# Performance work log

Hardware: AMD Instinct MI355X
Metric: run time of the kernel (lower is better)

The kernel has to match this reference:

```python
import jax, jax.numpy as jnp
import numpy as np

N = 250000   # num nodes
E = 250000   # num edges (tree: ~one parent per node)
D = 128      # embed_size
H = 256      # MLP hidden
HOPS = 3


def _mlp(x, w1, b1, w2, b2):
    # Sequential(Linear, ReLU, Linear, ReLU, Dropout(eval=identity))
    return jax.nn.relu(jnp.dot(jax.nn.relu(jnp.dot(x, w1) + b1), w2) + b2)


def _scatter_mean(src, idx, n):
    s = jax.ops.segment_sum(src, idx, num_segments=n)
    c = jax.ops.segment_sum(jnp.ones((src.shape[0],), src.dtype), idx, num_segments=n)
    return s / jnp.maximum(c, 1.0)[:, None]


def setup_inputs() -> dict:
    key = jax.random.key(0)
    ks = jax.random.split(key, 32)
    u = lambda k, shp: jax.random.uniform(k, shp, jnp.float32, -0.1, 0.1)
    inp = {
        "batch_token": jax.random.normal(ks[0], (N, D), jnp.float32),
        "self_idx_batch": jax.random.randint(ks[1], (E,), 0, N),
        "parent_idx_batch": jax.random.randint(ks[2], (E,), 0, N),
        "root_mask": (jax.random.uniform(ks[3], (N,)) < 0.01).astype(jnp.float32),
        "leaf_mask": (jax.random.uniform(ks[4], (N,)) < 0.3).astype(jnp.float32),
        "start_token": jax.random.normal(ks[5], (D,), jnp.float32),
        "end_token": jax.random.normal(ks[6], (D,), jnp.float32),
        # MLP_V: D -> H -> D
        "Vw1": u(ks[7], (D, H)), "Vb1": u(ks[8], (H,)), "Vw2": u(ks[9], (H, D)), "Vb2": u(ks[10], (D,)),
        # MLP_E: 1 -> H -> D
        "Ew1": u(ks[11], (1, H)), "Eb1": u(ks[12], (H,)), "Ew2": u(ks[13], (H, D)), "Eb2": u(ks[14], (D,)),
        # MLP_p: 3D -> H -> D
        "Pw1": u(ks[15], (3 * D, H)), "Pb1": u(ks[16], (H,)), "Pw2": u(ks[17], (H, D)), "Pb2": u(ks[18], (D,)),
        # MLP_c: 3D -> H -> D
        "Cw1": u(ks[19], (3 * D, H)), "Cb1": u(ks[20], (H,)), "Cw2": u(ks[21], (H, D)), "Cb2": u(ks[22], (D,)),
        # MLP_aggr: 3D -> H -> D
        "Aw1": u(ks[23], (3 * D, H)), "Ab1": u(ks[24], (H,)), "Aw2": u(ks[25], (H, D)), "Ab2": u(ks[26], (D,)),
    }
    return inp


def reference(batch_token, self_idx_batch, parent_idx_batch, root_mask, leaf_mask,
              start_token, end_token,
              Vw1, Vb1, Vw2, Vb2,
              Ew1, Eb1, Ew2, Eb2,
              Pw1, Pb1, Pw2, Pb2,
              Cw1, Cb1, Cw2, Cb2,
              Aw1, Ab1, Aw2, Ab2):
    n = batch_token.shape[0]
    edge_in = _mlp(jnp.ones((1, 1), batch_token.dtype), Ew1, Eb1, Ew2, Eb2)   # [1,D]
    edge_out = _mlp(jnp.zeros((1, 1), batch_token.dtype), Ew1, Eb1, Ew2, Eb2)  # [1,D]
    e = self_idx_batch.shape[0]
    edge_in = jnp.broadcast_to(edge_in, (e, edge_in.shape[1]))
    edge_out = jnp.broadcast_to(edge_out, (e, edge_out.shape[1]))

    hidden = _mlp(batch_token, Vw1, Vb1, Vw2, Vb2)  # [N,D]
    for _ in range(HOPS):
        node_self = hidden[self_idx_batch]      # [E,D] gather
        node_parent = hidden[parent_idx_batch]  # [E,D] gather
        inp_parent = jnp.concatenate([node_parent, node_self, edge_out], axis=-1)  # [E,3D]
        inp_child = jnp.concatenate([node_self, node_parent, edge_in], axis=-1)    # [E,3D]
        S_p = _mlp(inp_parent, Pw1, Pb1, Pw2, Pb2)
        S_c = _mlp(inp_child, Cw1, Cb1, Cw2, Cb2)
        S_p = _scatter_mean(S_p, self_idx_batch, n)
        S_c = _scatter_mean(S_c, parent_idx_batch, n)
        S_p = S_p + root_mask[:, None] * start_token
        S_c = S_c + leaf_mask[:, None] * end_token
        x_aggr = jnp.concatenate([hidden, S_p, S_c], axis=-1)  # [N,3D]
        hidden = hidden + _mlp(x_aggr, Aw1, Ab1, Aw2, Ab2)
    return hidden
```

## Files before the change

### kernel.cpp

```cpp
#include <hip/hip_runtime.h>

typedef __attribute__((ext_vector_type(8))) short short8;
typedef __attribute__((ext_vector_type(4))) float f32x4;

#define DD 128
#define HH 256

__device__ __forceinline__ unsigned short f2bf(float f) {
  unsigned int u = __float_as_uint(f);
  u += 0x7fffu + ((u >> 16) & 1u);
  return (unsigned short)(u >> 16);
}
__device__ __forceinline__ float bf2f(unsigned short s) {
  return __uint_as_float(((unsigned int)s) << 16);
}
__device__ __forceinline__ f32x4 mfma16(short8 a, short8 b, f32x4 c) {
  return __builtin_amdgcn_mfma_f32_16x16x32_bf16(a, b, c, 0, 0, 0);
}

__global__ void wconv(const float* __restrict__ src, unsigned short* __restrict__ dst,
                      int K, int Nout, int kswap) {
  int id = blockIdx.x * 256 + threadIdx.x;
  if (id >= K * Nout) return;
  int n = id / K, k = id - n * K;
  int ks = k + kswap; if (ks >= K) ks -= K;
  dst[n * K + k] = f2bf(src[(size_t)ks * Nout + n]);
}

__global__ void prep_bias(const float* __restrict__ Ew1, const float* __restrict__ Eb1,
                          const float* __restrict__ Ew2, const float* __restrict__ Eb2,
                          const float* __restrict__ Pw1, const float* __restrict__ Pb1,
                          const float* __restrict__ Cw1, const float* __restrict__ Cb1,
                          float* __restrict__ b1P, float* __restrict__ b1C) {
  __shared__ float h1[HH], h0[HH], ein[DD], eout[DD];
  int t = threadIdx.x;
  h1[t] = fmaxf(Ew1[t] + Eb1[t], 0.f);
  h0[t] = fmaxf(Eb1[t], 0.f);
  __syncthreads();
  if (t < DD) {
    float s1 = Eb2[t], s0 = Eb2[t];
    for (int j = 0; j < HH; ++j) { s1 += h1[j] * Ew2[j * DD + t]; s0 += h0[j] * Ew2[j * DD + t]; }
    ein[t]  = fmaxf(s1, 0.f);
    eout[t] = fmaxf(s0, 0.f);
  }
  __syncthreads();
  float bp = Pb1[t], bc = Cb1[t];
  for (int d = 0; d < DD; ++d) {
    bp += eout[d] * Pw1[(size_t)(256 + d) * HH + t];
    bc += ein[d]  * Cw1[(size_t)(256 + d) * HH + t];
  }
  b1P[t] = bp; b1C[t] = bc;
}

__global__ void count_k(const int* __restrict__ selfI, const int* __restrict__ parI,
                        int* degP, int* degC, int E) {
  int id = blockIdx.x * 256 + threadIdx.x;
  if (id < E) { atomicAdd(&degP[selfI[id]], 1); atomicAdd(&degC[parI[id]], 1); }
}

__global__ void scan1(const int* __restrict__ src, int* __restrict__ dst,
                      int* __restrict__ part, int n) {
  __shared__ int sh[256];
  int t = threadIdx.x;
  int base = blockIdx.x * 1024 + t * 4;
  int v0 = base + 0 < n ? src[base + 0] : 0;
  int v1 = base + 1 < n ? src[base + 1] : 0;
  int v2 = base + 2 < n ? src[base + 2] : 0;
  int v3 = base + 3 < n ? src[base + 3] : 0;
  int tsum = v0 + v1 + v2 + v3;
  sh[t] = tsum;
  __syncthreads();
  for (int off = 1; off < 256; off <<= 1) {
    int y = (t >= off) ? sh[t - off] : 0;
    __syncthreads();
    if (t >= off) sh[t] += y;
    __syncthreads();
  }
  int ex = sh[t] - tsum;
  if (base + 0 < n) dst[base + 0] = ex;
  if (base + 1 < n) dst[base + 1] = ex + v0;
  if (base + 2 < n) dst[base + 2] = ex + v0 + v1;
  if (base + 3 < n) dst[base + 3] = ex + v0 + v1 + v2;
  if (t == 255) part[blockIdx.x] = sh[255];
}

__global__ void scan2(int* __restrict__ part, int m) {
  __shared__ int sh[256];
  int t = threadIdx.x;
  int carry = 0;
  for (int base = 0; base < m; base += 256) {
    int v = (base + t < m) ? part[base + t] : 0;
    sh[t] = v;
    __syncthreads();
    for (int off = 1; off < 256; off <<= 1) {
      int y = (t >= off) ? sh[t - off] : 0;
      __syncthreads();
      if (t >= off) sh[t] += y;
      __syncthreads();
    }
    if (base + t < m) part[base + t] = carry + sh[t] - v;
    int tot = sh[255];
    __syncthreads();
    carry += tot;
  }
}

__global__ void scan3(int* __restrict__ dst, const int* __restrict__ part, int n) {
  int i = blockIdx.x * 256 + threadIdx.x;
  if (i < n) dst[i] += part[i >> 10];
}

__global__ void copy2(const int* __restrict__ a, int* __restrict__ b,
                      const int* __restrict__ c, int* __restrict__ d, int n) {
  int i = blockIdx.x * 256 + threadIdx.x;
  if (i < n) { b[i] = a[i]; d[i] = c[i]; }
}

__global__ void pos_k(const int* __restrict__ selfI, const int* __restrict__ parI,
                      int* curP, int* curC, int* posP, int* posC, int E) {
  int e = blockIdx.x * 256 + threadIdx.x;
  if (e < E) {
    posP[e] = atomicAdd(&curP[selfI[e]], 1);
    posC[e] = atomicAdd(&curC[parI[e]], 1);
  }
}

__global__ __launch_bounds__(512, 4) void v_kernel(
    const float* __restrict__ x, const unsigned short* __restrict__ W1t,
    const unsigned short* __restrict__ W2t, const float* __restrict__ b1,
    const float* __restrict__ b2, float* __restrict__ hidden,
    unsigned short* __restrict__ hbf, int n) {
  __shared__ __align__(16) unsigned short A[64 * 136];
  __shared__ __align__(16) unsigned short O1[64 * 264];
  int t = threadIdx.x;
  int w = t >> 6, lane = t & 63, ln = lane & 15, quad = lane >> 4, qo = quad * 8;
  long tile0 = (long)blockIdx.x * 64;
  int rl = t >> 3, part = t & 7;
  int c0 = part * 16;
  long gr = tile0 + rl;
  const float* src = x + (size_t)(gr < n ? gr : 0) * DD + c0;
  unsigned short* arow = A + rl * 136 + c0;
#pragma unroll
  for (int i = 0; i < 4; ++i) {
    float4 v = *(const float4*)(src + i * 4);
    *(ushort4*)(arow + i * 4) = make_ushort4(f2bf(v.x), f2bf(v.y), f2bf(v.z), f2bf(v.w));
  }
  __syncthreads();
  f32x4 acc[4][2];
#pragma unroll
  for (int m = 0; m < 4; ++m) {
    acc[m][0] = {0.f, 0.f, 0.f, 0.f}; acc[m][1] = {0.f, 0.f, 0.f, 0.f};
  }
#pragma unroll
  for (int kt = 0; kt < 4; ++kt) {
    short8 a[4];
#pragma unroll
    for (int m = 0; m < 4; ++m)
      a[m] = *(const short8*)(A + (m * 16 + ln) * 136 + kt * 32 + qo);
#pragma unroll
    for (int nn = 0; nn < 2; ++nn) {
      short8 b = *(const short8*)(W1t + (size_t)(w * 32 + nn * 16 + ln) * 128 + kt * 32 + qo);
#pragma unroll
      for (int m = 0; m < 4; ++m) acc[m][nn] = mfma16(a[m], b, acc[m][nn]);
    }
  }
#pragma unroll
  for (int nn = 0; nn < 2; ++nn) {
    int col = w * 32 + nn * 16 + ln;
    float bb = b1[col];
#pragma unroll
    for (int m = 0; m < 4; ++m)
#pragma unroll
      for (int r = 0; r < 4; ++r)
        O1[(m * 16 + quad * 4 + r) * 264 + col] = f2bf(fmaxf(acc[m][nn][r] + bb, 0.f));
  }
  __syncthreads();
  f32x4 acc2[4];
#pragma unroll
  for (int m = 0; m < 4; ++m) acc2[m] = {0.f, 0.f, 0.f, 0.f};
#pragma unroll
  for (int kt = 0; kt < 8; ++kt) {
    short8 b = *(const short8*)(W2t + (size_t)(w * 16 + ln) * 256 + kt * 32 + qo);
#pragma unroll
    for (int m = 0; m < 4; ++m) {
      short8 a = *(const short8*)(O1 + (m * 16 + ln) * 264 + kt * 32 + qo);
      acc2[m] = mfma16(a, b, acc2[m]);
    }
  }
  {
    int col = w * 16 + ln;
    float bb = b2[col];
#pragma unroll
    for (int m = 0; m < 4; ++m)
#pragma unroll
      for (int r = 0; r < 4; ++r) {
        long gr2 = tile0 + m * 16 + quad * 4 + r;
        if (gr2 < n) {
          float v = fmaxf(acc2[m][r] + bb, 0.f);
          hidden[gr2 * DD + col] = v;
          if (hbf) hbf[gr2 * DD + col] = f2bf(v);
        }
      }
  }
}

__global__ __launch_bounds__(512, 4) void edge_kernel(
    const float* __restrict__ hidden, const unsigned short* __restrict__ hbf,
    const int* __restrict__ selfI, const int* __restrict__ parI,
    const int* __restrict__ posP, const int* __restrict__ posC,
    const unsigned short* __restrict__ Pw1t, const unsigned short* __restrict__ Pw2t,
    const unsigned short* __restrict__ Cw1t, const unsigned short* __restrict__ Cw2t,
    const float* __restrict__ b1P, const float* __restrict__ b1C,
    const float* __restrict__ b2P, const float* __restrict__ b2C,
    unsigned short* __restrict__ SpE, unsigned short* __restrict__ ScE, int E) {
  __shared__ __align__(16) unsigned short A[64 * 264];
  __shared__ __align__(16) unsigned short O1[64 * 264];
  int t = threadIdx.x;
  int w = t >> 6, lane = t & 63, ln = lane & 15, quad = lane >> 4, qo = quad * 8;
  long tile0 = (long)blockIdx.x * 64;
  int rl = t >> 3, part = t & 7;
  long ge = tile0 + rl;
  bool vrow = ge < E;
  int si = vrow ? selfI[ge] : 0;
  int pi = vrow ? parI[ge] : 0;
  unsigned short* dstA = A + rl * 264 + part * 32;
  if (hbf) {
    const unsigned short* srcb = (part < 4) ? (hbf + (size_t)si * DD + part * 32)
                                            : (hbf + (size_t)pi * DD + (part - 4) * 32);
#pragma unroll
    for (int i = 0; i < 4; ++i)
      *(short8*)(dstA + i * 8) = *(const short8*)(srcb + i * 8);
  } else {
    const float* src = (part < 4) ? (hidden + (size_t)si * DD + part * 32)
                                  : (hidden + (size_t)pi * DD + (part - 4) * 32);
#pragma unroll
    for (int i = 0; i < 8; ++i) {
      float4 v = *(const float4*)(src + i * 4);
      *(ushort4*)(dstA + i * 4) = make_ushort4(f2bf(v.x), f2bf(v.y), f2bf(v.z), f2bf(v.w));
    }
  }
  __syncthreads();

  f32x4 accP[4][2], accC[4][2];
#pragma unroll
  for (int m = 0; m < 4; ++m) {
    accP[m][0] = {0.f, 0.f, 0.f, 0.f}; accP[m][1] = {0.f, 0.f, 0.f, 0.f};
    accC[m][0] = {0.f, 0.f, 0.f, 0.f}; accC[m][1] = {0.f, 0.f, 0.f, 0.f};
  }
#pragma unroll
  for (int kt = 0; kt < 8; ++kt) {
    short8 a[4];
#pragma unroll
    for (int m = 0; m < 4; ++m)
      a[m] = *(const short8*)(A + (m * 16 + ln) * 264 + kt * 32 + qo);
#pragma unroll
    for (int nn = 0; nn < 2; ++nn) {
      short8 bp = *(const short8*)(Pw1t + (size_t)(w * 32 + nn * 16 + ln) * 256 + kt * 32 + qo);
      short8 bc = *(const short8*)(Cw1t + (size_t)(w * 32 + nn * 16 + ln) * 256 + kt * 32 + qo);
#pragma unroll
      for (int m = 0; m < 4; ++m) {
        accP[m][nn] = mfma16(a[m], bp, accP[m][nn]);
        accC[m][nn] = mfma16(a[m], bc, accC[m][nn]);
      }
    }
  }

#pragma unroll
  for (int mlp = 0; mlp < 2; ++mlp) {
    const unsigned short* W2t = mlp ? Cw2t : Pw2t;
    const float* b1 = mlp ? b1C : b1P;
    const float* b2 = mlp ? b2C : b2P;
    unsigned short* Sout = mlp ? ScE : SpE;
    const int* pos = mlp ? posC : posP;
#pragma unroll
    for (int nn = 0; nn < 2; ++nn) {
      int col = w * 32 + nn * 16 + ln;
      float bb = b1[col];
#pragma unroll
      for (int m = 0; m < 4; ++m)
#pragma unroll
        for (int r = 0; r < 4; ++r) {
          float v = mlp ? accC[m][nn][r] : accP[m][nn][r];
          O1[(m * 16 + quad * 4 + r) * 264 + col] = f2bf(fmaxf(v + bb, 0.f));
        }
    }
    __syncthreads();
    f32x4 acc2[4];
#pragma unroll
    for (int m = 0; m < 4; ++m) acc2[m] = {0.f, 0.f, 0.f, 0.f};
#pragma unroll
    for (int kt = 0; kt < 8; ++kt) {
      short8 b = *(const short8*)(W2t + (size_t)(w * 16 + ln) * 256 + kt * 32 + qo);
#pragma unroll
      for (int m = 0; m < 4; ++m) {
        short8 a = *(const short8*)(O1 + (m * 16 + ln) * 264 + kt * 32 + qo);
        acc2[m] = mfma16(a, b, acc2[m]);
      }
    }
    __syncthreads();
    {
      int col = w * 16 + ln;
      float bb = b2[col];
#pragma unroll
      for (int m = 0; m < 4; ++m)
#pragma unroll
        for (int r = 0; r < 4; ++r)
          O1[(m * 16 + quad * 4 + r) * 264 + col] = f2bf(fmaxf(acc2[m][r] + bb, 0.f));
    }
    __syncthreads();
    if (vrow) {
      int dpos = pos[ge];
      const unsigned short* srow = O1 + rl * 264 + part * 16;
      ushort4* dst = (ushort4*)(Sout + (size_t)dpos * DD + part * 16);
#pragma unroll
      for (int i = 0; i < 4; ++i) dst[i] = *(const ushort4*)(srow + i * 4);
    }
    __syncthreads();
  }
}

__global__ __launch_bounds__(512, 4) void node_kernel(
    float* __restrict__ hidden, unsigned short* __restrict__ hbf,
    const unsigned short* __restrict__ SpE, const unsigned short* __restrict__ ScE,
    const int* __restrict__ offP, const int* __restrict__ degP,
    const int* __restrict__ offC, const int* __restrict__ degC,
    const float* __restrict__ rootM, const float* __restrict__ leafM,
    const float* __restrict__ startT, const float* __restrict__ endT,
    const unsigned short* __restrict__ W1t, const unsigned short* __restrict__ W2t,
    const float* __restrict__ b1, const float* __restrict__ b2, int n) {
  __shared__ __align__(16) unsigned short A[64 * 392];
  int t = threadIdx.x;
  int w = t >> 6, lane = t & 63, ln = lane & 15, quad = lane >> 4, qo = quad * 8;
  long tile0 = (long)blockIdx.x * 64;
  int rl = t >> 3, part = t & 7;
  int c0 = part * 16;
  long gr = tile0 + rl;
  long g = (gr < n) ? gr : 0;
  unsigned short* arow = A + rl * 392;
  if (hbf) {
    const unsigned short* hrowb = hbf + (size_t)g * DD + c0;
    *(short8*)(arow + c0)     = *(const short8*)(hrowb);
    *(short8*)(arow + c0 + 8) = *(const short8*)(hrowb + 8);
  } else {
    const float* hrow = hidden + (size_t)g * DD + c0;
#pragma unroll
    for (int i = 0; i < 4; ++i) {
      float4 h = *(const float4*)(hrow + i * 4);
      *(ushort4*)(arow + c0 + i * 4) = make_ushort4(f2bf(h.x), f2bf(h.y), f2bf(h.z), f2bf(h.w));
    }
  }
  {
    int off = offP[g], dg = degP[g];
    float s[16];
#pragma unroll
    for (int i = 0; i < 16; ++i) s[i] = 0.f;
    for (int j = 0; j < dg; ++j) {
      const unsigned short* rr = SpE + (size_t)(off + j) * DD + c0;
#pragma unroll
      for (int i = 0; i < 4; ++i) {
        ushort4 u = *(const ushort4*)(rr + i * 4);
        s[i * 4 + 0] += bf2f(u.x); s[i * 4 + 1] += bf2f(u.y);
        s[i * 4 + 2] += bf2f(u.z); s[i * 4 + 3] += bf2f(u.w);
      }
    }
    float ip = 1.f / fmaxf((float)dg, 1.f);
    float rm = rootM[g];
#pragma unroll
    for (int i = 0; i < 4; ++i) {
      float4 st = *(const float4*)(startT + c0 + i * 4);
      *(ushort4*)(arow + 128 + c0 + i * 4) = make_ushort4(
          f2bf(s[i * 4 + 0] * ip + rm * st.x), f2bf(s[i * 4 + 1] * ip + rm * st.y),
          f2bf(s[i * 4 + 2] * ip + rm * st.z), f2bf(s[i * 4 + 3] * ip + rm * st.w));
    }
  }
  {
    int off = offC[g], dg = degC[g];
    float s[16];
#pragma unroll
    for (int i = 0; i < 16; ++i) s[i] = 0.f;
    for (int j = 0; j < dg; ++j) {
      const unsigned short* rr = ScE + (size_t)(off + j) * DD + c0;
#pragma unroll
      for (int i = 0; i < 4; ++i) {
        ushort4 u = *(const ushort4*)(rr + i * 4);
        s[i * 4 + 0] += bf2f(u.x); s[i * 4 + 1] += bf2f(u.y);
        s[i * 4 + 2] += bf2f(u.z); s[i * 4 + 3] += bf2f(u.w);
      }
    }
    float ic = 1.f / fmaxf((float)dg, 1.f);
    float lm = leafM[g];
#pragma unroll
    for (int i = 0; i < 4; ++i) {
      float4 et = *(const float4*)(endT + c0 + i * 4);
      *(ushort4*)(arow + 256 + c0 + i * 4) = make_ushort4(
          f2bf(s[i * 4 + 0] * ic + lm * et.x), f2bf(s[i * 4 + 1] * ic + lm * et.y),
          f2bf(s[i * 4 + 2] * ic + lm * et.z), f2bf(s[i * 4 + 3] * ic + lm * et.w));
    }
  }
  __syncthreads();
  f32x4 acc[4][2];
#pragma unroll
  for (int m = 0; m < 4; ++m) {
    acc[m][0] = {0.f, 0.f, 0.f, 0.f}; acc[m][1] = {0.f, 0.f, 0.f, 0.f};
  }
#pragma unroll
  for (int kt = 0; kt < 12; ++kt) {
    short8 a[4];
#pragma unroll
    for (int m = 0; m < 4; ++m)
      a[m] = *(const short8*)(A + (m * 16 + ln) * 392 + kt * 32 + qo);
#pragma unroll
    for (int nn = 0; nn < 2; ++nn) {
      short8 b = *(const short8*)(W1t + (size_t)(w * 32 + nn * 16 + ln) * 384 + kt * 32 + qo);
#pragma unroll
      for (int m = 0; m < 4; ++m) acc[m][nn] = mfma16(a[m], b, acc[m][nn]);
    }
  }
  __syncthreads();
#pragma unroll
  for (int nn = 0; nn < 2; ++nn) {
    int col = w * 32 + nn * 16 + ln;
    float bb = b1[col];
#pragma unroll
    for (int m = 0; m < 4; ++m)
#pragma unroll
      for (int r = 0; r < 4; ++r)
        A[(m * 16 + quad * 4 + r) * 392 + col] = f2bf(fmaxf(acc[m][nn][r] + bb, 0.f));
  }
  __syncthreads();
  f32x4 acc2[4];
#pragma unroll
  for (int m = 0; m < 4; ++m) acc2[m] = {0.f, 0.f, 0.f, 0.f};
#pragma unroll
  for (int kt = 0; kt < 8; ++kt) {
    short8 b = *(const short8*)(W2t + (size_t)(w * 16 + ln) * 256 + kt * 32 + qo);
#pragma unroll
    for (int m = 0; m < 4; ++m) {
      short8 a = *(const short8*)(A + (m * 16 + ln) * 392 + kt * 32 + qo);
      acc2[m] = mfma16(a, b, acc2[m]);
    }
  }
  __syncthreads();
  {
    int col = w * 16 + ln;
    float bb = b2[col];
#pragma unroll
    for (int m = 0; m < 4; ++m)
#pragma unroll
      for (int r = 0; r < 4; ++r)
        ((float*)(A + (size_t)(m * 16 + quad * 4 + r) * 392))[col] =
            fmaxf(acc2[m][r] + bb, 0.f);
  }
  __syncthreads();
  if (gr < n) {
    const float* F = (const float*)(A + (size_t)rl * 392);
    float* hrow = hidden + (size_t)gr * DD + c0;
    unsigned short* brow = hbf ? hbf + (size_t)gr * DD + c0 : nullptr;
#pragma unroll
    for (int i = 0; i < 4; ++i) {
      float4 v = *(const float4*)(F + c0 + i * 4);
      float4 h = *(const float4*)(hrow + i * 4);
      h.x += v.x; h.y += v.y; h.z += v.z; h.w += v.w;
      *(float4*)(hrow + i * 4) = h;
      if (brow)
        *(ushort4*)(brow + i * 4) = make_ushort4(f2bf(h.x), f2bf(h.y), f2bf(h.z), f2bf(h.w));
    }
  }
}

extern "C" void kernel_launch(void* const* d_in, const int* in_sizes, int n_in,
                              void* d_out, int out_size, void* d_ws, size_t ws_size,
                              hipStream_t stream) {
  const float* batch  = (const float*)d_in[0];
  const int*   selfI  = (const int*)d_in[1];
  const int*   parI   = (const int*)d_in[2];
  const float* rootM  = (const float*)d_in[3];
  const float* leafM  = (const float*)d_in[4];
  const float* startT = (const float*)d_in[5];
  const float* endT   = (const float*)d_in[6];
  const float* Vw1 = (const float*)d_in[7],  *Vb1 = (const float*)d_in[8];
  const float* Vw2 = (const float*)d_in[9],  *Vb2 = (const float*)d_in[10];
  const float* Ew1 = (const float*)d_in[11], *Eb1 = (const float*)d_in[12];
  const float* Ew2 = (const float*)d_in[13], *Eb2 = (const float*)d_in[14];
  const float* Pw1 = (const float*)d_in[15], *Pb1 = (const float*)d_in[16];
  const float* Pw2 = (const float*)d_in[17], *Pb2 = (const float*)d_in[18];
  const float* Cw1 = (const float*)d_in[19], *Cb1 = (const float*)d_in[20];
  const float* Cw2 = (const float*)d_in[21], *Cb2 = (const float*)d_in[22];
  const float* Aw1 = (const float*)d_in[23], *Ab1 = (const float*)d_in[24];
  const float* Aw2 = (const float*)d_in[25], *Ab2 = (const float*)d_in[26];

  const int N = in_sizes[3];
  const int E = in_sizes[1];
  float* out = (float*)d_out;

  char* p = (char*)d_ws;
  auto nxt = [&](size_t sz) { char* r = p; p += (sz + 255) & ~(size_t)255; return r; };
  unsigned short* SpE = (unsigned short*)nxt((size_t)E * DD * 2);
  unsigned short* ScE = (unsigned short*)nxt((size_t)E * DD * 2);
  int* degP = (int*)nxt((size_t)N * 4);
  int* degC = (int*)nxt((size_t)N * 4);
  int* offP = (int*)nxt((size_t)N * 4);
  int* offC = (int*)nxt((size_t)N * 4);
  int* curP = (int*)nxt((size_t)N * 4);
  int* curC = (int*)nxt((size_t)N * 4);
  int* posP = (int*)nxt((size_t)E * 4);
  int* posC = (int*)nxt((size_t)E * 4);
  int* partA = (int*)nxt(4096);
  int* partB = (int*)nxt(4096);
  unsigned short* Vw1t = (unsigned short*)nxt((size_t)128 * 256 * 2);
  unsigned short* Vw2t = (unsigned short*)nxt((size_t)256 * 128 * 2);
  unsigned short* Pw1t = (unsigned short*)nxt((size_t)256 * 256 * 2);
  unsigned short* Pw2t = (unsigned short*)nxt((size_t)256 * 128 * 2);
  unsigned short* Cw1t = (unsigned short*)nxt((size_t)256 * 256 * 2);
  unsigned short* Cw2t = (unsigned short*)nxt((size_t)256 * 128 * 2);
  unsigned short* Aw1t = (unsigned short*)nxt((size_t)384 * 256 * 2);
  unsigned short* Aw2t = (unsigned short*)nxt((size_t)256 * 128 * 2);
  float* b1P = (float*)nxt(256 * 4);
  float* b1C = (float*)nxt(256 * 4);
  unsigned short* Hbf = (unsigned short*)nxt((size_t)N * DD * 2);
  if ((size_t)(p - (char*)d_ws) > ws_size) Hbf = nullptr;

  hipMemsetAsync(degP, 0, (size_t)N * 4, stream);
  hipMemsetAsync(degC, 0, (size_t)N * 4, stream);

  auto blk = [](int total) { return dim3((total + 255) / 256); };
  wconv<<<blk(128 * 256), 256, 0, stream>>>(Vw1, Vw1t, 128, 256, 0);
  wconv<<<blk(256 * 128), 256, 0, stream>>>(Vw2, Vw2t, 256, 128, 0);
  wconv<<<blk(256 * 256), 256, 0, stream>>>(Pw1, Pw1t, 256, 256, 128);
  wconv<<<blk(256 * 128), 256, 0, stream>>>(Pw2, Pw2t, 256, 128, 0);
  wconv<<<blk(256 * 256), 256, 0, stream>>>(Cw1, Cw1t, 256, 256, 0);
  wconv<<<blk(256 * 128), 256, 0, stream>>>(Cw2, Cw2t, 256, 128, 0);
  wconv<<<blk(384 * 256), 256, 0, stream>>>(Aw1, Aw1t, 384, 256, 0);
  wconv<<<blk(256 * 128), 256, 0, stream>>>(Aw2, Aw2t, 256, 128, 0);

  prep_bias<<<1, 256, 0, stream>>>(Ew1, Eb1, Ew2, Eb2, Pw1, Pb1, Cw1, Cb1, b1P, b1C);
  count_k<<<blk(E), 256, 0, stream>>>(selfI, parI, degP, degC, E);

  int NB = (N + 1023) / 1024;
  scan1<<<NB, 256, 0, stream>>>(degP, offP, partA, N);
  scan1<<<NB, 256, 0, stream>>>(degC, offC, partB, N);
  scan2<<<1, 256, 0, stream>>>(partA, NB);
  scan2<<<1, 256, 0, stream>>>(partB, NB);
  scan3<<<blk(N), 256, 0, stream>>>(offP, partA, N);
  scan3<<<blk(N), 256, 0, stream>>>(offC, partB, N);
  copy2<<<blk(N), 256, 0, stream>>>(offP, curP, offC, curC, N);
  pos_k<<<blk(E), 256, 0, stream>>>(selfI, parI, curP, curC, posP, posC, E);

  dim3 gN((N + 63) / 64), gE((E + 63) / 64);
  v_kernel<<<gN, 512, 0, stream>>>(batch, Vw1t, Vw2t, Vb1, Vb2, out, Hbf, N);

  for (int hop = 0; hop < 3; ++hop) {
    edge_kernel<<<gE, 512, 0, stream>>>(out, Hbf, selfI, parI, posP, posC,
                                        Pw1t, Pw2t, Cw1t, Cw2t, b1P, b1C, Pb2, Cb2,
                                        SpE, ScE, E);
    node_kernel<<<gN, 512, 0, stream>>>(out, Hbf, SpE, ScE, offP, degP, offC, degC,
                                        rootM, leafM, startT, endT,
                                        Aw1t, Aw2t, Ab1, Ab2, N);
  }
}
```

Baseline: 1.883 ms.

## Sort edges by self index and merge setup kernels

Edges are permuted into CSR order by self index once during setup, so the edge kernel reads self/parent indices sequentially. Its S_p output is then written contiguously and the self-row gathers have locality. The weight conversion, scan and copy kernels are merged into fewer launches to cut launch overhead. This adds one reorder pass and three extra index arrays in workspace.

```diff
diff --git a/kernel.cpp b/kernel.cpp
--- a/kernel.cpp
+++ b/kernel.cpp
@@ -18,11 +18,27 @@
   return __builtin_amdgcn_mfma_f32_16x16x32_bf16(a, b, c, 0, 0, 0);
 }
 
-__global__ void wconv(const float* __restrict__ src, unsigned short* __restrict__ dst,
-                      int K, int Nout, int kswap) {
+__global__ void wconv_all(const float* __restrict__ s0, const float* __restrict__ s1,
+                          const float* __restrict__ s2, const float* __restrict__ s3,
+                          const float* __restrict__ s4, const float* __restrict__ s5,
+                          const float* __restrict__ s6, const float* __restrict__ s7,
+                          unsigned short* __restrict__ d0, unsigned short* __restrict__ d1,
+                          unsigned short* __restrict__ d2, unsigned short* __restrict__ d3,
+                          unsigned short* __restrict__ d4, unsigned short* __restrict__ d5,
+                          unsigned short* __restrict__ d6, unsigned short* __restrict__ d7) {
   int id = blockIdx.x * 256 + threadIdx.x;
-  if (id >= K * Nout) return;
-  int n = id / K, k = id - n * K;
+  const float* src; unsigned short* dst; int K, Nout, kswap = 0, base;
+  if (id < 32768)       { src = s0; dst = d0; K = 128; Nout = 256; base = 0; }
+  else if (id < 65536)  { src = s1; dst = d1; K = 256; Nout = 128; base = 32768; }
+  else if (id < 131072) { src = s2; dst = d2; K = 256; Nout = 256; base = 65536; kswap = 128; }
+  else if (id < 163840) { src = s3; dst = d3; K = 256; Nout = 128; base = 131072; }
+  else if (id < 229376) { src = s4; dst = d4; K = 256; Nout = 256; base = 163840; }
+  else if (id < 262144) { src = s5; dst = d5; K = 256; Nout = 128; base = 229376; }
+  else if (id < 360448) { src = s6; dst = d6; K = 384; Nout = 256; base = 262144; }
+  else if (id < 393216) { src = s7; dst = d7; K = 256; Nout = 128; base = 360448; }
+  else return;
+  int lid = id - base;
+  int n = lid / K, k = lid - n * K;
   int ks = k + kswap; if (ks >= K) ks -= K;
   dst[n * K + k] = f2bf(src[(size_t)ks * Nout + n]);
 }
@@ -58,8 +74,12 @@
   if (id < E) { atomicAdd(&degP[selfI[id]], 1); atomicAdd(&degC[parI[id]], 1); }
 }
 
-__global__ void scan1(const int* __restrict__ src, int* __restrict__ dst,
-                      int* __restrict__ part, int n) {
+__global__ void scan1_2(const int* __restrict__ srcA, int* __restrict__ dstA, int* __restrict__ partA,
+                        const int* __restrict__ srcB, int* __restrict__ dstB, int* __restrict__ partB,
+                        int n) {
+  const int* src = blockIdx.y ? srcB : srcA;
+  int* dst = blockIdx.y ? dstB : dstA;
+  int* part = blockIdx.y ? partB : partA;
   __shared__ int sh[256];
   int t = threadIdx.x;
   int base = blockIdx.x * 1024 + t * 4;
@@ -84,7 +104,8 @@
   if (t == 255) part[blockIdx.x] = sh[255];
 }
 
-__global__ void scan2(int* __restrict__ part, int m) {
+__global__ void scan2_2(int* __restrict__ partA, int* __restrict__ partB, int m) {
+  int* part = blockIdx.x ? partB : partA;
   __shared__ int sh[256];
   int t = threadIdx.x;
   int carry = 0;
@@ -105,15 +126,16 @@
   }
 }
 
-__global__ void scan3(int* __restrict__ dst, const int* __restrict__ part, int n) {
+__global__ void scan3copy(int* __restrict__ offP, const int* __restrict__ partA, int* __restrict__ curP,
+                          int* __restrict__ offC, const int* __restrict__ partB, int* __restrict__ curC,
+                          int n) {
   int i = blockIdx.x * 256 + threadIdx.x;
-  if (i < n) dst[i] += part[i >> 10];
-}
-
-__global__ void copy2(const int* __restrict__ a, int* __restrict__ b,
-                      const int* __restrict__ c, int* __restrict__ d, int n) {
-  int i = blockIdx.x * 256 + threadIdx.x;
-  if (i < n) { b[i] = a[i]; d[i] = c[i]; }
+  if (i < n) {
+    int a = offP[i] + partA[i >> 10];
+    int b = offC[i] + partB[i >> 10];
+    offP[i] = a; curP[i] = a;
+    offC[i] = b; curC[i] = b;
+  }
 }
 
 __global__ void pos_k(const int* __restrict__ selfI, const int* __restrict__ parI,
@@ -122,6 +144,19 @@
   if (e < E) {
     posP[e] = atomicAdd(&curP[selfI[e]], 1);
     posC[e] = atomicAdd(&curC[parI[e]], 1);
+  }
+}
+
+__global__ void reorder_k(const int* __restrict__ selfI, const int* __restrict__ parI,
+                          const int* __restrict__ posP, const int* __restrict__ posC,
+                          int* __restrict__ selfS, int* __restrict__ parS,
+                          int* __restrict__ posCS, int E) {
+  int e = blockIdx.x * 256 + threadIdx.x;
+  if (e < E) {
+    int slot = posP[e];
+    selfS[slot] = selfI[e];
+    parS[slot] = parI[e];
+    posCS[slot] = posC[e];
   }
 }
 
@@ -206,8 +241,8 @@
 
 __global__ __launch_bounds__(512, 4) void edge_kernel(
     const float* __restrict__ hidden, const unsigned short* __restrict__ hbf,
-    const int* __restrict__ selfI, const int* __restrict__ parI,
-    const int* __restrict__ posP, const int* __restrict__ posC,
+    const int* __restrict__ selfS, const int* __restrict__ parS,
+    const int* __restrict__ posCS,
     const unsigned short* __restrict__ Pw1t, const unsigned short* __restrict__ Pw2t,
     const unsigned short* __restrict__ Cw1t, const unsigned short* __restrict__ Cw2t,
     const float* __restrict__ b1P, const float* __restrict__ b1C,
@@ -221,8 +256,8 @@
   int rl = t >> 3, part = t & 7;
   long ge = tile0 + rl;
   bool vrow = ge < E;
-  int si = vrow ? selfI[ge] : 0;
-  int pi = vrow ? parI[ge] : 0;
+  int si = vrow ? selfS[ge] : 0;
+  int pi = vrow ? parS[ge] : 0;
   unsigned short* dstA = A + rl * 264 + part * 32;
   if (hbf) {
     const unsigned short* srcb = (part < 4) ? (hbf + (size_t)si * DD + part * 32)
@@ -271,7 +306,6 @@
     const float* b1 = mlp ? b1C : b1P;
     const float* b2 = mlp ? b2C : b2P;
     unsigned short* Sout = mlp ? ScE : SpE;
-    const int* pos = mlp ? posC : posP;
 #pragma unroll
     for (int nn = 0; nn < 2; ++nn) {
       int col = w * 32 + nn * 16 + ln;
@@ -309,9 +343,9 @@
     }
     __syncthreads();
     if (vrow) {
-      int dpos = pos[ge];
+      size_t dpos = mlp ? (size_t)posCS[ge] : (size_t)ge;
       const unsigned short* srow = O1 + rl * 264 + part * 16;
-      ushort4* dst = (ushort4*)(Sout + (size_t)dpos * DD + part * 16);
+      ushort4* dst = (ushort4*)(Sout + dpos * DD + part * 16);
 #pragma unroll
       for (int i = 0; i < 4; ++i) dst[i] = *(const ushort4*)(srow + i * 4);
     }
@@ -505,6 +539,9 @@
   int* curC = (int*)nxt((size_t)N * 4);
   int* posP = (int*)nxt((size_t)E * 4);
   int* posC = (int*)nxt((size_t)E * 4);
+  int* selfS = (int*)nxt((size_t)E * 4);
+  int* parS = (int*)nxt((size_t)E * 4);
+  int* posCS = (int*)nxt((size_t)E * 4);
   int* partA = (int*)nxt(4096);
   int* partB = (int*)nxt(4096);
   unsigned short* Vw1t = (unsigned short*)nxt((size_t)128 * 256 * 2);
@@ -524,33 +561,24 @@
   hipMemsetAsync(degC, 0, (size_t)N * 4, stream);
 
   auto blk = [](int total) { return dim3((total + 255) / 256); };
-  wconv<<<blk(128 * 256), 256, 0, stream>>>(Vw1, Vw1t, 128, 256, 0);
-  wconv<<<blk(256 * 128), 256, 0, stream>>>(Vw2, Vw2t, 256, 128, 0);
-  wconv<<<blk(256 * 256), 256, 0, stream>>>(Pw1, Pw1t, 256, 256, 128);
-  wconv<<<blk(256 * 128), 256, 0, stream>>>(Pw2, Pw2t, 256, 128, 0);
-  wconv<<<blk(256 * 256), 256, 0, stream>>>(Cw1, Cw1t, 256, 256, 0);
-  wconv<<<blk(256 * 128), 256, 0, stream>>>(Cw2, Cw2t, 256, 128, 0);
-  wconv<<<blk(384 * 256), 256, 0, stream>>>(Aw1, Aw1t, 384, 256, 0);
-  wconv<<<blk(256 * 128), 256, 0, stream>>>(Aw2, Aw2t, 256, 128, 0);
+  wconv_all<<<blk(393216), 256, 0, stream>>>(Vw1, Vw2, Pw1, Pw2, Cw1, Cw2, Aw1, Aw2,
+                                             Vw1t, Vw2t, Pw1t, Pw2t, Cw1t, Cw2t, Aw1t, Aw2t);
 
   prep_bias<<<1, 256, 0, stream>>>(Ew1, Eb1, Ew2, Eb2, Pw1, Pb1, Cw1, Cb1, b1P, b1C);
   count_k<<<blk(E), 256, 0, stream>>>(selfI, parI, degP, degC, E);
 
   int NB = (N + 1023) / 1024;
-  scan1<<<NB, 256, 0, stream>>>(degP, offP, partA, N);
-  scan1<<<NB, 256, 0, stream>>>(degC, offC, partB, N);
-  scan2<<<1, 256, 0, stream>>>(partA, NB);
-  scan2<<<1, 256, 0, stream>>>(partB, NB);
-  scan3<<<blk(N), 256, 0, stream>>>(offP, partA, N);
-  scan3<<<blk(N), 256, 0, stream>>>(offC, partB, N);
-  copy2<<<blk(N), 256, 0, stream>>>(offP, curP, offC, curC, N);
+  scan1_2<<<dim3(NB, 2), 256, 0, stream>>>(degP, offP, partA, degC, offC, partB, N);
+  scan2_2<<<2, 256, 0, stream>>>(partA, partB, NB);
+  scan3copy<<<blk(N), 256, 0, stream>>>(offP, partA, curP, offC, partB, curC, N);
   pos_k<<<blk(E), 256, 0, stream>>>(selfI, parI, curP, curC, posP, posC, E);
+  reorder_k<<<blk(E), 256, 0, stream>>>(selfI, parI, posP, posC, selfS, parS, posCS, E);
 
   dim3 gN((N + 63) / 64), gE((E + 63) / 64);
   v_kernel<<<gN, 512, 0, stream>>>(batch, Vw1t, Vw2t, Vb1, Vb2, out, Hbf, N);
 
   for (int hop = 0; hop < 3; ++hop) {
-    edge_kernel<<<gE, 512, 0, stream>>>(out, Hbf, selfI, parI, posP, posC,
+    edge_kernel<<<gE, 512, 0, stream>>>(out, Hbf, selfS, parS, posCS,
                                         Pw1t, Pw2t, Cw1t, Cw2t, b1P, b1C, Pb2, Cb2,
                                         SpE, ScE, E);
     node_kernel<<<gN, 512, 0, stream>>>(out, Hbf, SpE, ScE, offP, degP, offC, degC,
```

Result: faster. 1.841 ms (-2.2%).
